# Kernel tuning notes

Hardware: AMD Instinct MI355X
Metric: run time of the kernel (lower is better)

## Reference

```python
import jax, jax.numpy as jnp
import numpy as np

B, SQ, SK, D = 4, 2048, 2048, 1024


def setup_inputs() -> dict:
    key = jax.random.key(0)
    ks = jax.random.split(key, 8)
    s = 1.0 / np.sqrt(D)
    return {
        "input_seq": jax.random.normal(ks[0], (B, SQ, D), jnp.float32),
        "condition_seq": jax.random.normal(ks[1], (B, SK, D), jnp.float32),
        "Wq": jax.random.normal(ks[2], (D, D), jnp.float32) * s,
        "bq": jnp.zeros((D,), jnp.float32),
        "Wk": jax.random.normal(ks[3], (D, D), jnp.float32) * s,
        "bk": jnp.zeros((D,), jnp.float32),
        "Wv": jax.random.normal(ks[4], (D, D), jnp.float32) * s,
        "bv": jnp.zeros((D,), jnp.float32),
    }


def reference(input_seq, condition_seq, Wq, bq, Wk, bk, Wv, bv):
    # Linear projections (torch Linear: x @ W.T + b)
    q = jnp.einsum("bsd,ed->bse", input_seq, Wq) + bq        # [B,SQ,D]
    k = jnp.einsum("btd,ed->bte", condition_seq, Wk) + bk    # [B,SK,D]
    v = jnp.einsum("btd,ed->bte", condition_seq, Wv) + bv    # [B,SK,D]
    # NOTE: original module omits the 1/sqrt(d) scaling — kept faithful.
    scores = jnp.einsum("bse,bte->bst", q, k)                # [B,SQ,SK]
    attn = jax.nn.softmax(scores, axis=-1)
    attended = jnp.einsum("bst,bte->bse", attn, v)           # [B,SQ,D]
    return attended
```

## Files before the change

### kernel.cpp

```cpp
#include <hip/hip_runtime.h>

using f32x4  = __attribute__((ext_vector_type(4))) float;
using bf16x8 = __attribute__((ext_vector_type(8))) __bf16;
using f16x8  = __attribute__((ext_vector_type(8))) _Float16;
using u16x4  = __attribute__((ext_vector_type(4))) unsigned short;
using u16x8  = __attribute__((ext_vector_type(8))) unsigned short;

constexpr int Bb = 4, SQn = 2048, SKn = 2048, Dd = 1024;

__device__ __forceinline__ unsigned fbitsu(float x){ union{float f;unsigned u;}c; c.f=x; return c.u; }
__device__ __forceinline__ float ubitsf(unsigned u){ union{unsigned u;float f;}c; c.u=u; return c.f; }
__device__ __forceinline__ unsigned short hi_trunc(float x){ return (unsigned short)(fbitsu(x)>>16); }
__device__ __forceinline__ unsigned short hi_rne(float x){ unsigned u=fbitsu(x); return (unsigned short)((u + 0x7FFFu + ((u>>16)&1u))>>16); }
__device__ __forceinline__ float from_hi(unsigned short h){ return ubitsf(((unsigned)h)<<16); }
__device__ __forceinline__ unsigned short h_rne(float x){ _Float16 h = (_Float16)x; return __builtin_bit_cast(unsigned short, h); }
__device__ __forceinline__ float h2f(unsigned short u){ return (float)__builtin_bit_cast(_Float16, u); }

template<int DT> __device__ __forceinline__ unsigned short cvt_rne(float x){ return DT ? h_rne(x) : hi_rne(x); }
template<int DT> __device__ __forceinline__ float cvt_f(unsigned short u){ return DT ? h2f(u) : from_hi(u); }

__device__ __forceinline__ f32x4 mfma_bf16(bf16x8 a, bf16x8 b, f32x4 c){
    return __builtin_amdgcn_mfma_f32_16x16x32_bf16(a, b, c, 0, 0, 0);
}
__device__ __forceinline__ f32x4 mfma_f16(u16x8 a, u16x8 b, f32x4 c){
    return __builtin_amdgcn_mfma_f32_16x16x32_f16(
        __builtin_bit_cast(f16x8, a), __builtin_bit_cast(f16x8, b), c, 0, 0, 0);
}
template<int DT>
__device__ __forceinline__ f32x4 mfma_u16(u16x8 a, u16x8 b, f32x4 c){
    if constexpr (DT) return mfma_f16(a, b, c);
    else return __builtin_amdgcn_mfma_f32_16x16x32_bf16(
        __builtin_bit_cast(bf16x8, a), __builtin_bit_cast(bf16x8, b), c, 0, 0, 0);
}

__device__ __forceinline__ void gload16(const void* g, void* l){
    __builtin_amdgcn_global_load_lds(
        (const __attribute__((address_space(1))) unsigned int*)g,
        (__attribute__((address_space(3))) unsigned int*)l, 16, 0, 0);
}

__device__ __forceinline__ void xcd_swz(int& bx, int& by){
    const int nx = gridDim.x, nwg = nx * gridDim.y;
    int l = by * nx + bx;
    l = (l & 7) * (nwg >> 3) + (l >> 3);
    bx = l % nx; by = l / nx;
}

__global__ __launch_bounds__(256)
void split2(const float* __restrict__ x, const float* __restrict__ c,
            unsigned short* __restrict__ xh, unsigned short* __restrict__ xl,
            unsigned short* __restrict__ ch, unsigned short* __restrict__ cl,
            int n4)
{
    const int stride = gridDim.x * 256;
    for (int i = blockIdx.x * 256 + threadIdx.x; i < 2 * n4; i += stride) {
        const bool second = (i >= n4);
        const int j = second ? i - n4 : i;
        const float* in = second ? c : x;
        unsigned short* hi = second ? ch : xh;
        unsigned short* lo = second ? cl : xl;
        float a[4]; *(float4*)a = *(const float4*)(in + (size_t)j * 4);
        u16x4 h, l;
#pragma unroll
        for (int r = 0; r < 4; ++r) {
            h[r] = h_rne(a[r]);
            l[r] = h_rne(a[r] - h2f(h[r]));
        }
        *(u16x4*)&hi[(size_t)j * 4] = h;
        *(u16x4*)&lo[(size_t)j * 4] = l;
    }
}

template<int TERMS, int BM_, int BN_, int BK_, int EPI, int DT>
__global__ __launch_bounds__(256, 2)
void gemm_tile(const unsigned short* __restrict__ Ahg, const unsigned short* __restrict__ Alg,
               const unsigned short* __restrict__ Bhg, const unsigned short* __restrict__ Blg,
               void* __restrict__ O0v, void* __restrict__ O1v,
               int M, int N, int K, long aBS, long bBS, long oBS)
{
    constexpr int ROWB = BK_ * 2;
    constexpr int RPC  = 1024 / ROWB;
    constexpr int CA   = BM_ / RPC;
    constexpr int CB   = BN_ / RPC;
    constexpr int AI   = BM_ / 32;
    constexpr int BJ   = BN_ / 32;
    constexpr int KH   = BK_ / 32;
    static_assert(CA % 4 == 0 && CB % 4 == 0, "chunks divisible by 4 waves");

    __shared__ __align__(16) unsigned short Ash[BM_*BK_], Bsh[BN_*BK_];
    __shared__ __align__(16) unsigned short Asl[TERMS>=2?BM_*BK_:8];
    __shared__ __align__(16) unsigned short Bsl[TERMS==3?BN_*BK_:8];

    const int z = blockIdx.z;
    Ahg += (size_t)z * aBS;
    Bhg += (size_t)z * bBS;
    if (TERMS >= 2) Alg += (size_t)z * aBS;
    if (TERMS == 3) Blg += (size_t)z * bBS;

    int bx = blockIdx.x, by = blockIdx.y;
    xcd_swz(bx, by);

    const int tid = threadIdx.x, lane = tid & 63, w = tid >> 6;
    const int wr = (w >> 1) * (BM_/2), wc = (w & 1) * (BN_/2);
    const int lr = lane & 15, lg = lane >> 4;
    const int m0 = by * BM_, n0 = bx * BN_;
    constexpr int rsh = (ROWB == 64) ? 2 : 3;
    const int rowc = lane >> rsh;
    const int colb = (lane & ((1 << rsh) - 1)) << 4;
    const size_t rsBy = (size_t)K * 2;

    f32x4 acc[AI][BJ] = {};

    for (int k0 = 0; k0 < K; k0 += BK_) {
#pragma unroll
        for (int c4 = 0; c4 < CA/4; ++c4) {
            const int c = c4*4 + w;
            const size_t go = (size_t)(m0 + c*RPC + rowc) * rsBy + (size_t)k0*2 + colb;
            gload16((const char*)Ahg + go, (char*)Ash + c*1024);
            if (TERMS >= 2) gload16((const char*)Alg + go, (char*)Asl + c*1024);
        }
#pragma unroll
        for (int c4 = 0; c4 < CB/4; ++c4) {
            const int c = c4*4 + w;
            const size_t go = (size_t)(n0 + c*RPC + rowc) * rsBy + (size_t)k0*2 + colb;
            gload16((const char*)Bhg + go, (char*)Bsh + c*1024);
            if (TERMS == 3) gload16((const char*)Blg + go, (char*)Bsl + c*1024);
        }
        __syncthreads();

#pragma unroll
        for (int kk = 0; kk < KH; ++kk) {
            u16x8 ah[AI], bh[BJ];
#pragma unroll
            for (int i = 0; i < AI; ++i) ah[i] = *(const u16x8*)&Ash[(wr + i*16 + lr)*BK_ + kk*32 + lg*8];
#pragma unroll
            for (int j = 0; j < BJ; ++j) bh[j] = *(const u16x8*)&Bsh[(wc + j*16 + lr)*BK_ + kk*32 + lg*8];
            if (TERMS == 3) {
                u16x8 al[AI], bl[BJ];
#pragma unroll
                for (int i = 0; i < AI; ++i) al[i] = *(const u16x8*)&Asl[(wr + i*16 + lr)*BK_ + kk*32 + lg*8];
#pragma unroll
                for (int j = 0; j < BJ; ++j) bl[j] = *(const u16x8*)&Bsl[(wc + j*16 + lr)*BK_ + kk*32 + lg*8];
#pragma unroll
                for (int i = 0; i < AI; ++i)
#pragma unroll
                    for (int j = 0; j < BJ; ++j) {
                        acc[i][j] = mfma_u16<DT>(ah[i], bh[j], acc[i][j]);
                        acc[i][j] = mfma_u16<DT>(ah[i], bl[j], acc[i][j]);
                        acc[i][j] = mfma_u16<DT>(al[i], bh[j], acc[i][j]);
                    }
            } else if (TERMS == 2) {
                u16x8 al[AI];
#pragma unroll
                for (int i = 0; i < AI; ++i) al[i] = *(const u16x8*)&Asl[(wr + i*16 + lr)*BK_ + kk*32 + lg*8];
#pragma unroll
                for (int i = 0; i < AI; ++i)
#pragma unroll
                    for (int j = 0; j < BJ; ++j) {
                        acc[i][j] = mfma_u16<DT>(ah[i], bh[j], acc[i][j]);
                        acc[i][j] = mfma_u16<DT>(al[i], bh[j], acc[i][j]);
                    }
            } else {
#pragma unroll
                for (int i = 0; i < AI; ++i)
#pragma unroll
                    for (int j = 0; j < BJ; ++j)
                        acc[i][j] = mfma_u16<DT>(ah[i], bh[j], acc[i][j]);
            }
        }
        __syncthreads();
    }

    if (EPI == 0) {
        float* C = (float*)O0v + (size_t)z * oBS;
#pragma unroll
        for (int j = 0; j < BJ; ++j) {
            const int col = n0 + wc + j*16 + lr;
#pragma unroll
            for (int i = 0; i < AI; ++i)
#pragma unroll
                for (int r = 0; r < 4; ++r)
                    C[(size_t)(m0 + wr + i*16 + lg*4 + r) * N + col] = acc[i][j][r];
        }
    } else {
        unsigned short* Chi = (unsigned short*)O0v + (size_t)z * oBS;
        unsigned short* Clo = (unsigned short*)O1v + (size_t)z * oBS;
#pragma unroll
        for (int j = 0; j < BJ; ++j) {
            const int col = n0 + wc + j*16 + lr;
#pragma unroll
            for (int i = 0; i < AI; ++i)
#pragma unroll
                for (int r = 0; r < 4; ++r) {
                    const size_t idx = (size_t)(m0 + wr + i*16 + lg*4 + r) * N + col;
                    const float v = acc[i][j][r];
                    const unsigned short h = cvt_rne<DT>(v);
                    Chi[idx] = h;
                    Clo[idx] = cvt_rne<DT>(v - cvt_f<DT>(h));
                }
        }
    }
}

template<int EPI>
__global__ __launch_bounds__(256, 2)
void gemm_mixed(const unsigned short* __restrict__ Ahg, const unsigned short* __restrict__ Alg,
                const float* __restrict__ Bw, const float* __restrict__ bias,
                unsigned short* __restrict__ O0, unsigned short* __restrict__ O1,
                int M, int N, int K)
{
    constexpr int BM_ = 128, BN_ = 128, BK_ = 32;
    __shared__ __align__(16) unsigned short Ash[BM_*BK_], Asl[BM_*BK_];
    __shared__ __align__(16) unsigned short Bsh[BN_*BK_];

    int bx = blockIdx.x, by = blockIdx.y;
    xcd_swz(bx, by);

    const int tid = threadIdx.x, lane = tid & 63, w = tid >> 6;
    const int wr = (w >> 1) * 64, wc = (w & 1) * 64;
    const int lr = lane & 15, lg = lane >> 4;
    const int m0 = by * BM_, n0 = bx * BN_;
    const int rowc = lane >> 2;
    const int colb = (lane & 3) << 4;
    const size_t rsBy = (size_t)K * 2;

    f32x4 acc[4][4] = {};

    for (int k0 = 0; k0 < K; k0 += BK_) {
        float4 bv[4];
#pragma unroll
        for (int u = 0; u < 4; ++u) {
            const int f = u*256 + tid;
            bv[u] = *(const float4*)(Bw + (size_t)(n0 + (f >> 3))*K + k0 + ((f & 7) << 2));
        }
        __syncthreads();

#pragma unroll
        for (int c4 = 0; c4 < 2; ++c4) {
            const int c = c4*4 + w;
            const size_t go = (size_t)(m0 + c*16 + rowc) * rsBy + (size_t)k0*2 + colb;
            gload16((const char*)Ahg + go, (char*)Ash + c*1024);
            gload16((const char*)Alg + go, (char*)Asl + c*1024);
        }
#pragma unroll
        for (int u = 0; u < 4; ++u) {
            const int f = u*256 + tid;
            const int row = f >> 3, ko = (f & 7) << 2;
            float b4[4]; *(float4*)b4 = bv[u];
            u16x4 bh;
#pragma unroll
            for (int r = 0; r < 4; ++r) bh[r] = h_rne(b4[r]);
            *(u16x4*)&Bsh[row*BK_ + ko] = bh;
        }
        __syncthreads();

        u16x8 ah[4], al[4], bh[4];
#pragma unroll
        for (int i = 0; i < 4; ++i) {
            ah[i] = *(const u16x8*)&Ash[(wr + i*16 + lr)*BK_ + lg*8];
            al[i] = *(const u16x8*)&Asl[(wr + i*16 + lr)*BK_ + lg*8];
        }
#pragma unroll
        for (int j = 0; j < 4; ++j) bh[j] = *(const u16x8*)&Bsh[(wc + j*16 + lr)*BK_ + lg*8];
#pragma unroll
        for (int i = 0; i < 4; ++i)
#pragma unroll
            for (int j = 0; j < 4; ++j) {
                acc[i][j] = mfma_f16(ah[i], bh[j], acc[i][j]);
                acc[i][j] = mfma_f16(al[i], bh[j], acc[i][j]);
            }
    }

#pragma unroll
    for (int j = 0; j < 4; ++j) {
        const int col = n0 + wc + j*16 + lr;
        const float bc = bias[col];
#pragma unroll
        for (int i = 0; i < 4; ++i) {
            if (EPI == 0) {
#pragma unroll
                for (int r = 0; r < 4; ++r) {
                    const int row = m0 + wr + i*16 + lg*4 + r;
                    const float v = acc[i][j][r] + bc;
                    const unsigned short h = h_rne(v);
                    O0[(size_t)row*N + col] = h;
                    O1[(size_t)row*N + col] = h_rne(v - h2f(h));
                }
            } else if (EPI == 2) {
#pragma unroll
                for (int r = 0; r < 4; ++r) {
                    const int row = m0 + wr + i*16 + lg*4 + r;
                    O0[(size_t)row*N + col] = h_rne(acc[i][j][r] + bc);
                }
            } else {
                const int row0 = m0 + wr + i*16 + lg*4;
                const int b = row0 >> 11, t0 = row0 & 2047;
                u16x4 pk;
#pragma unroll
                for (int r = 0; r < 4; ++r) pk[r] = h_rne(acc[i][j][r] + bc);
                *(u16x4*)&O0[(((size_t)b*Dd + col) << 11) + t0] = pk;
            }
        }
    }
}

template<int TERMS, int EPI>
__global__ __launch_bounds__(256, 2)
void gemm_proj(const float* __restrict__ A, const float* __restrict__ Bm,
               const float* __restrict__ bias,
               unsigned short* __restrict__ O0, unsigned short* __restrict__ O1,
               int M, int N, int K)
{
    constexpr int BM_ = 128, BN_ = 64, BK_ = 32;
    __shared__ __align__(16) unsigned short Ash[BM_*BK_], Bsh[BN_*BK_];
    __shared__ __align__(16) unsigned short Asl[TERMS==3?BM_*BK_:8], Bsl[TERMS==3?BN_*BK_:8];

    const int tid = threadIdx.x, lane = tid & 63, w = tid >> 6;
    const int wr = (w >> 1) * 64, wc = (w & 1) * 32;
    const int lr = lane & 15, lg = lane >> 4;
    const int m0 = blockIdx.y * BM_, n0 = blockIdx.x * BN_;

    f32x4 acc[4][2] = {};

    for (int k0 = 0; k0 < K; k0 += BK_) {
        float4 av[4], bv[2];
#pragma unroll
        for (int u = 0; u < 4; ++u) {
            const int f = u*256 + tid;
            av[u] = *(const float4*)(A + (size_t)(m0 + (f >> 3))*K + k0 + ((f & 7) << 2));
        }
#pragma unroll
        for (int u = 0; u < 2; ++u) {
            const int f = u*256 + tid;
            bv[u] = *(const float4*)(Bm + (size_t)(n0 + (f >> 3))*K + k0 + ((f & 7) << 2));
        }
        __syncthreads();
#pragma unroll
        for (int u = 0; u < 4; ++u) {
            const int f = u*256 + tid;
            const int row = f >> 3, ko = (f & 7) << 2;
            float a4[4]; *(float4*)a4 = av[u];
            u16x4 ah;
            if (TERMS == 3) {
                u16x4 al;
#pragma unroll
                for (int j = 0; j < 4; ++j) { ah[j] = hi_trunc(a4[j]); al[j] = hi_trunc(a4[j] - from_hi(ah[j])); }
                *(u16x4*)&Asl[row*BK_ + ko] = al;
            } else {
#pragma unroll
                for (int j = 0; j < 4; ++j) ah[j] = hi_rne(a4[j]);
            }
            *(u16x4*)&Ash[row*BK_ + ko] = ah;
        }
#pragma unroll
        for (int u = 0; u < 2; ++u) {
            const int f = u*256 + tid;
            const int row = f >> 3, ko = (f & 7) << 2;
            float b4[4]; *(float4*)b4 = bv[u];
            u16x4 bh;
            if (TERMS == 3) {
                u16x4 bl;
#pragma unroll
                for (int j = 0; j < 4; ++j) { bh[j] = hi_trunc(b4[j]); bl[j] = hi_trunc(b4[j] - from_hi(bh[j])); }
                *(u16x4*)&Bsl[row*BK_ + ko] = bl;
            } else {
#pragma unroll
                for (int j = 0; j < 4; ++j) bh[j] = hi_rne(b4[j]);
            }
            *(u16x4*)&Bsh[row*BK_ + ko] = bh;
        }
        __syncthreads();

        bf16x8 ah[4], bh[2];
#pragma unroll
        for (int i = 0; i < 4; ++i) ah[i] = *(const bf16x8*)&Ash[(wr + i*16 + lr)*BK_ + lg*8];
#pragma unroll
        for (int j = 0; j < 2; ++j) bh[j] = *(const bf16x8*)&Bsh[(wc + j*16 + lr)*BK_ + lg*8];
        if (TERMS == 3) {
            bf16x8 al[4], bl[2];
#pragma unroll
            for (int i = 0; i < 4; ++i) al[i] = *(const bf16x8*)&Asl[(wr + i*16 + lr)*BK_ + lg*8];
#pragma unroll
            for (int j = 0; j < 2; ++j) bl[j] = *(const bf16x8*)&Bsl[(wc + j*16 + lr)*BK_ + lg*8];
#pragma unroll
            for (int i = 0; i < 4; ++i)
#pragma unroll
                for (int j = 0; j < 2; ++j) {
                    acc[i][j] = mfma_bf16(ah[i], bh[j], acc[i][j]);
                    acc[i][j] = mfma_bf16(ah[i], bl[j], acc[i][j]);
                    acc[i][j] = mfma_bf16(al[i], bh[j], acc[i][j]);
                }
        } else {
#pragma unroll
            for (int i = 0; i < 4; ++i)
#pragma unroll
                for (int j = 0; j < 2; ++j)
                    acc[i][j] = mfma_bf16(ah[i], bh[j], acc[i][j]);
        }
        __syncthreads();
    }

#pragma unroll
    for (int j = 0; j < 2; ++j) {
        const int col = n0 + wc + j*16 + lr;
        const float bc = bias[col];
#pragma unroll
        for (int i = 0; i < 4; ++i) {
            if (EPI == 0) {
#pragma unroll
                for (int r = 0; r < 4; ++r) {
                    const int row = m0 + wr + i*16 + lg*4 + r;
                    const float v = acc[i][j][r] + bc;
                    const unsigned short h = h_rne(v);
                    O0[(size_t)row*N + col] = h;
                    O1[(size_t)row*N + col] = h_rne(v - h2f(h));
                }
            } else if (EPI == 2) {
#pragma unroll
                for (int r = 0; r < 4; ++r) {
                    const int row = m0 + wr + i*16 + lg*4 + r;
                    O0[(size_t)row*N + col] = h_rne(acc[i][j][r] + bc);
                }
            } else {
                const int row0 = m0 + wr + i*16 + lg*4;
                const int b = row0 >> 11, t0 = row0 & 2047;
                u16x4 pk;
#pragma unroll
                for (int r = 0; r < 4; ++r) pk[r] = h_rne(acc[i][j][r] + bc);
                *(u16x4*)&O0[(((size_t)b*Dd + col) << 11) + t0] = pk;
            }
        }
    }
}

__global__ __launch_bounds__(256)
void softmax_sp(unsigned short* __restrict__ Shi, const unsigned short* __restrict__ Slo)
{
    const int tid = threadIdx.x;
    unsigned short* ph = Shi + (size_t)blockIdx.x * SKn;
    const unsigned short* pl = Slo + (size_t)blockIdx.x * SKn;
    __shared__ float red[8];

    u16x4 h0 = *(const u16x4*)&ph[tid*4];
    u16x4 h1 = *(const u16x4*)&ph[1024 + tid*4];
    u16x4 l0 = *(const u16x4*)&pl[tid*4];
    u16x4 l1 = *(const u16x4*)&pl[1024 + tid*4];
    float v[8];
#pragma unroll
    for (int r = 0; r < 4; ++r) {
        v[r]   = h2f(h0[r]) + h2f(l0[r]);
        v[4+r] = h2f(h1[r]) + h2f(l1[r]);
    }
    float m = v[0];
#pragma unroll
    for (int r = 1; r < 8; ++r) m = fmaxf(m, v[r]);
#pragma unroll
    for (int o2 = 32; o2 > 0; o2 >>= 1) m = fmaxf(m, __shfl_down(m, o2));
    if ((tid & 63) == 0) red[tid >> 6] = m;
    __syncthreads();
    m = fmaxf(fmaxf(red[0],red[1]), fmaxf(red[2],red[3]));

    float e[8], s = 0.f;
#pragma unroll
    for (int r = 0; r < 8; ++r) { e[r] = __expf(v[r] - m); s += e[r]; }
#pragma unroll
    for (int o2 = 32; o2 > 0; o2 >>= 1) s += __shfl_down(s, o2);
    if ((tid & 63) == 0) red[4 + (tid >> 6)] = s;
    __syncthreads();
    const float inv = 1.f / ((red[4]+red[5])+(red[6]+red[7]));

    u16x4 p0, p1;
#pragma unroll
    for (int r = 0; r < 4; ++r) { p0[r] = h_rne(e[r]*inv); p1[r] = h_rne(e[4+r]*inv); }
    *(u16x4*)&ph[tid*4] = p0;
    *(u16x4*)&ph[1024 + tid*4] = p1;
}

extern "C" void kernel_launch(void* const* d_in, const int* in_sizes, int n_in,
                              void* d_out, int out_size, void* d_ws, size_t ws_size,
                              hipStream_t stream)
{
    const float* x  = (const float*)d_in[0];
    const float* c  = (const float*)d_in[1];
    const float* Wq = (const float*)d_in[2];
    const float* bq = (const float*)d_in[3];
    const float* Wk = (const float*)d_in[4];
    const float* bk = (const float*)d_in[5];
    const float* Wv = (const float*)d_in[6];
    const float* bv = (const float*)d_in[7];
    float* out = (float*)d_out;

    const size_t nQ = (size_t)Bb * SQn * Dd;
    const size_t sE = (size_t)SQn * SKn;
    unsigned short* Qh = (unsigned short*)d_ws;
    unsigned short* Ql = Qh + nQ;
    unsigned short* Kh = Ql + nQ;
    unsigned short* Kl = Kh + nQ;
    unsigned short* Vt = Kl + nQ;
    unsigned short* Shi = Vt + nQ;
    unsigned short* Slo = Shi + (size_t)Bb * sE;

    unsigned short* xh = Shi;
    unsigned short* xl = Shi + nQ;
    unsigned short* ch = Slo;
    unsigned short* cl = Slo + nQ;

    const size_t needB = (size_t)(Shi - Qh) * 2 + (size_t)Bb * sE * 2 * 2;
    const bool batched = ws_size >= needB;

    const dim3 blk(256);

    if (batched) {
        split2<<<dim3(4096), blk, 0, stream>>>(x, c, xh, xl, ch, cl, (int)(nQ/4));

        const dim3 gp(Dd/128, (Bb*SQn)/128);
        gemm_mixed<0><<<gp, blk, 0, stream>>>(xh, xl, Wq, bq, Qh, Ql, Bb*SQn, Dd, Dd);
        gemm_mixed<2><<<gp, blk, 0, stream>>>(ch, cl, Wk, bk, Kh, nullptr, Bb*SKn, Dd, Dd);
        gemm_mixed<1><<<gp, blk, 0, stream>>>(ch, cl, Wv, bv, Vt, nullptr, Bb*SKn, Dd, Dd);

        gemm_tile<2,128,128,32,1,1><<<dim3(SKn/128, SQn/128, Bb), blk, 0, stream>>>(
            Qh, Ql, Kh, nullptr, Shi, Slo, SQn, SKn, Dd,
            (long)SQn*Dd, (long)SKn*Dd, (long)sE);
        softmax_sp<<<dim3(Bb*SQn), blk, 0, stream>>>(Shi, Slo);
        gemm_tile<1,128,128,32,0,1><<<dim3(Dd/128, SQn/128, Bb), blk, 0, stream>>>(
            Shi, nullptr, Vt, nullptr, out, nullptr, SQn, Dd, SKn,
            (long)sE, (long)Dd*SKn, (long)SQn*Dd);
    } else {
        unsigned short* ShiF = Shi;
        unsigned short* SloF = Shi + sE;
        gemm_proj<3,0><<<dim3(Dd/64, (Bb*SQn)/128), blk, 0, stream>>>(x, Wq, bq, Qh, Ql, Bb*SQn, Dd, Dd);
        gemm_proj<3,2><<<dim3(Dd/64, (Bb*SKn)/128), blk, 0, stream>>>(c, Wk, bk, Kh, nullptr, Bb*SKn, Dd, Dd);
        gemm_proj<1,1><<<dim3(Dd/64, (Bb*SKn)/128), blk, 0, stream>>>(c, Wv, bv, Vt, nullptr, Bb*SKn, Dd, Dd);
        for (int b = 0; b < Bb; ++b) {
            const size_t qoff = (size_t)b * SQn * Dd;
            const size_t koff = (size_t)b * SKn * Dd;
            gemm_tile<2,128,64,32,1,1><<<dim3(SKn/64, SQn/128, 1), blk, 0, stream>>>(
                Qh+qoff, Ql+qoff, Kh+koff, nullptr, ShiF, SloF, SQn, SKn, Dd, 0, 0, 0);
            softmax_sp<<<dim3(SQn), blk, 0, stream>>>(ShiF, SloF);
            gemm_tile<1,64,64,32,0,1><<<dim3(Dd/64, SQn/64, 1), blk, 0, stream>>>(
                ShiF, nullptr, Vt+(size_t)b*Dd*SKn, nullptr, out+qoff, nullptr,
                SQn, Dd, SKn, 0, 0, 0);
        }
    }
}
```

Measured before the change: 315.6 us.

## Pre-convert projection weights to fp16 once and fuse K/V projections into one kernel

A new cvtW kernel converts Wq, Wk and Wv to fp16 once, into workspace space reused from the unused Kl buffer. The projection GEMMs then load B tiles with async global-to-LDS copies instead of reloading fp32 weights and converting them in every tile. The Q projection now goes through the generic gemm_tile with a new bias epilogue. The K and V projections are fused into one gemm_kv kernel that loads the split condition tiles once and feeds both weight matrices, which doubles the accumulator registers and may reduce occupancy.

```diff
diff --git a/kernel.cpp b/kernel.cpp
--- a/kernel.cpp
+++ b/kernel.cpp
@@ -71,10 +71,31 @@
     }
 }
 
+__global__ __launch_bounds__(256)
+void cvtW(const float* __restrict__ Wq, const float* __restrict__ Wk,
+          const float* __restrict__ Wv,
+          unsigned short* __restrict__ oq, unsigned short* __restrict__ ok,
+          unsigned short* __restrict__ ov, int n4)
+{
+    const int stride = gridDim.x * 256;
+    for (int i = blockIdx.x * 256 + threadIdx.x; i < 3 * n4; i += stride) {
+        const float* src; unsigned short* dst; int j = i;
+        if (j < n4)          { src = Wq; dst = oq; }
+        else if (j < 2*n4)   { src = Wk; dst = ok; j -= n4; }
+        else                 { src = Wv; dst = ov; j -= 2*n4; }
+        float a[4]; *(float4*)a = *(const float4*)(src + (size_t)j * 4);
+        u16x4 h;
+#pragma unroll
+        for (int r = 0; r < 4; ++r) h[r] = h_rne(a[r]);
+        *(u16x4*)&dst[(size_t)j * 4] = h;
+    }
+}
+
 template<int TERMS, int BM_, int BN_, int BK_, int EPI, int DT>
 __global__ __launch_bounds__(256, 2)
 void gemm_tile(const unsigned short* __restrict__ Ahg, const unsigned short* __restrict__ Alg,
                const unsigned short* __restrict__ Bhg, const unsigned short* __restrict__ Blg,
+               const float* __restrict__ bias,
                void* __restrict__ O0v, void* __restrict__ O1v,
                int M, int N, int K, long aBS, long bBS, long oBS)
 {
@@ -188,12 +209,13 @@
 #pragma unroll
         for (int j = 0; j < BJ; ++j) {
             const int col = n0 + wc + j*16 + lr;
+            const float bc = (EPI == 2) ? bias[col] : 0.f;
 #pragma unroll
             for (int i = 0; i < AI; ++i)
 #pragma unroll
                 for (int r = 0; r < 4; ++r) {
                     const size_t idx = (size_t)(m0 + wr + i*16 + lg*4 + r) * N + col;
-                    const float v = acc[i][j][r];
+                    const float v = acc[i][j][r] + bc;
                     const unsigned short h = cvt_rne<DT>(v);
                     Chi[idx] = h;
                     Clo[idx] = cvt_rne<DT>(v - cvt_f<DT>(h));
@@ -202,16 +224,16 @@
     }
 }
 
-template<int EPI>
 __global__ __launch_bounds__(256, 2)
-void gemm_mixed(const unsigned short* __restrict__ Ahg, const unsigned short* __restrict__ Alg,
-                const float* __restrict__ Bw, const float* __restrict__ bias,
-                unsigned short* __restrict__ O0, unsigned short* __restrict__ O1,
-                int M, int N, int K)
+void gemm_kv(const unsigned short* __restrict__ Ahg, const unsigned short* __restrict__ Alg,
+             const unsigned short* __restrict__ Wk16, const unsigned short* __restrict__ Wv16,
+             const float* __restrict__ bk, const float* __restrict__ bv,
+             unsigned short* __restrict__ Kh, unsigned short* __restrict__ Vt,
+             int M, int N, int K)
 {
     constexpr int BM_ = 128, BN_ = 128, BK_ = 32;
     __shared__ __align__(16) unsigned short Ash[BM_*BK_], Asl[BM_*BK_];
-    __shared__ __align__(16) unsigned short Bsh[BN_*BK_];
+    __shared__ __align__(16) unsigned short Bks[BN_*BK_], Bvs[BN_*BK_];
 
     int bx = blockIdx.x, by = blockIdx.y;
     xcd_swz(bx, by);
@@ -224,82 +246,63 @@
     const int colb = (lane & 3) << 4;
     const size_t rsBy = (size_t)K * 2;
 
-    f32x4 acc[4][4] = {};
+    f32x4 acck[4][4] = {}, accv[4][4] = {};
 
     for (int k0 = 0; k0 < K; k0 += BK_) {
-        float4 bv[4];
-#pragma unroll
-        for (int u = 0; u < 4; ++u) {
-            const int f = u*256 + tid;
-            bv[u] = *(const float4*)(Bw + (size_t)(n0 + (f >> 3))*K + k0 + ((f & 7) << 2));
-        }
-        __syncthreads();
-
 #pragma unroll
         for (int c4 = 0; c4 < 2; ++c4) {
             const int c = c4*4 + w;
-            const size_t go = (size_t)(m0 + c*16 + rowc) * rsBy + (size_t)k0*2 + colb;
-            gload16((const char*)Ahg + go, (char*)Ash + c*1024);
-            gload16((const char*)Alg + go, (char*)Asl + c*1024);
-        }
-#pragma unroll
-        for (int u = 0; u < 4; ++u) {
-            const int f = u*256 + tid;
-            const int row = f >> 3, ko = (f & 7) << 2;
-            float b4[4]; *(float4*)b4 = bv[u];
-            u16x4 bh;
-#pragma unroll
-            for (int r = 0; r < 4; ++r) bh[r] = h_rne(b4[r]);
-            *(u16x4*)&Bsh[row*BK_ + ko] = bh;
-        }
-        __syncthreads();
-
-        u16x8 ah[4], al[4], bh[4];
+            const size_t goA = (size_t)(m0 + c*16 + rowc) * rsBy + (size_t)k0*2 + colb;
+            gload16((const char*)Ahg + goA, (char*)Ash + c*1024);
+            gload16((const char*)Alg + goA, (char*)Asl + c*1024);
+            const size_t goB = (size_t)(n0 + c*16 + rowc) * rsBy + (size_t)k0*2 + colb;
+            gload16((const char*)Wk16 + goB, (char*)Bks + c*1024);
+            gload16((const char*)Wv16 + goB, (char*)Bvs + c*1024);
+        }
+        __syncthreads();
+
+        u16x8 ah[4], al[4], bf[4];
 #pragma unroll
         for (int i = 0; i < 4; ++i) {
             ah[i] = *(const u16x8*)&Ash[(wr + i*16 + lr)*BK_ + lg*8];
             al[i] = *(const u16x8*)&Asl[(wr + i*16 + lr)*BK_ + lg*8];
         }
 #pragma unroll
-        for (int j = 0; j < 4; ++j) bh[j] = *(const u16x8*)&Bsh[(wc + j*16 + lr)*BK_ + lg*8];
+        for (int j = 0; j < 4; ++j) bf[j] = *(const u16x8*)&Bks[(wc + j*16 + lr)*BK_ + lg*8];
 #pragma unroll
         for (int i = 0; i < 4; ++i)
 #pragma unroll
             for (int j = 0; j < 4; ++j) {
-                acc[i][j] = mfma_f16(ah[i], bh[j], acc[i][j]);
-                acc[i][j] = mfma_f16(al[i], bh[j], acc[i][j]);
+                acck[i][j] = mfma_f16(ah[i], bf[j], acck[i][j]);
+                acck[i][j] = mfma_f16(al[i], bf[j], acck[i][j]);
             }
+#pragma unroll
+        for (int j = 0; j < 4; ++j) bf[j] = *(const u16x8*)&Bvs[(wc + j*16 + lr)*BK_ + lg*8];
+#pragma unroll
+        for (int i = 0; i < 4; ++i)
+#pragma unroll
+            for (int j = 0; j < 4; ++j) {
+                accv[i][j] = mfma_f16(ah[i], bf[j], accv[i][j]);
+                accv[i][j] = mfma_f16(al[i], bf[j], accv[i][j]);
+            }
+        __syncthreads();
     }
 
 #pragma unroll
     for (int j = 0; j < 4; ++j) {
         const int col = n0 + wc + j*16 + lr;
-        const float bc = bias[col];
+        const float bck = bk[col], bcv = bv[col];
 #pragma unroll
         for (int i = 0; i < 4; ++i) {
-            if (EPI == 0) {
-#pragma unroll
-                for (int r = 0; r < 4; ++r) {
-                    const int row = m0 + wr + i*16 + lg*4 + r;
-                    const float v = acc[i][j][r] + bc;
-                    const unsigned short h = h_rne(v);
-                    O0[(size_t)row*N + col] = h;
-                    O1[(size_t)row*N + col] = h_rne(v - h2f(h));
-                }
-            } else if (EPI == 2) {
-#pragma unroll
-                for (int r = 0; r < 4; ++r) {
-                    const int row = m0 + wr + i*16 + lg*4 + r;
-                    O0[(size_t)row*N + col] = h_rne(acc[i][j][r] + bc);
-                }
-            } else {
-                const int row0 = m0 + wr + i*16 + lg*4;
-                const int b = row0 >> 11, t0 = row0 & 2047;
-                u16x4 pk;
-#pragma unroll
-                for (int r = 0; r < 4; ++r) pk[r] = h_rne(acc[i][j][r] + bc);
-                *(u16x4*)&O0[(((size_t)b*Dd + col) << 11) + t0] = pk;
-            }
+            const int row0 = m0 + wr + i*16 + lg*4;
+#pragma unroll
+            for (int r = 0; r < 4; ++r)
+                Kh[(size_t)(row0 + r)*N + col] = h_rne(acck[i][j][r] + bck);
+            const int b = row0 >> 11, t0 = row0 & 2047;
+            u16x4 pk;
+#pragma unroll
+            for (int r = 0; r < 4; ++r) pk[r] = h_rne(accv[i][j][r] + bcv);
+            *(u16x4*)&Vt[(((size_t)b*Dd + col) << 11) + t0] = pk;
         }
     }
 }
@@ -492,6 +495,7 @@
 
     const size_t nQ = (size_t)Bb * SQn * Dd;
     const size_t sE = (size_t)SQn * SKn;
+    const size_t nW = (size_t)Dd * Dd;
     unsigned short* Qh = (unsigned short*)d_ws;
     unsigned short* Ql = Qh + nQ;
     unsigned short* Kh = Ql + nQ;
@@ -500,6 +504,10 @@
     unsigned short* Shi = Vt + nQ;
     unsigned short* Slo = Shi + (size_t)Bb * sE;
 
+    unsigned short* Wq16 = Kl;
+    unsigned short* Wk16 = Kl + nW;
+    unsigned short* Wv16 = Kl + 2*nW;
+
     unsigned short* xh = Shi;
     unsigned short* xl = Shi + nQ;
     unsigned short* ch = Slo;
@@ -512,18 +520,19 @@
 
     if (batched) {
         split2<<<dim3(4096), blk, 0, stream>>>(x, c, xh, xl, ch, cl, (int)(nQ/4));
-
-        const dim3 gp(Dd/128, (Bb*SQn)/128);
-        gemm_mixed<0><<<gp, blk, 0, stream>>>(xh, xl, Wq, bq, Qh, Ql, Bb*SQn, Dd, Dd);
-        gemm_mixed<2><<<gp, blk, 0, stream>>>(ch, cl, Wk, bk, Kh, nullptr, Bb*SKn, Dd, Dd);
-        gemm_mixed<1><<<gp, blk, 0, stream>>>(ch, cl, Wv, bv, Vt, nullptr, Bb*SKn, Dd, Dd);
+        cvtW<<<dim3(1024), blk, 0, stream>>>(Wq, Wk, Wv, Wq16, Wk16, Wv16, (int)(nW/4));
+
+        gemm_tile<2,128,128,32,2,1><<<dim3(Dd/128, (Bb*SQn)/128), blk, 0, stream>>>(
+            xh, xl, Wq16, nullptr, bq, Qh, Ql, Bb*SQn, Dd, Dd, 0, 0, 0);
+        gemm_kv<<<dim3(Dd/128, (Bb*SKn)/128), blk, 0, stream>>>(
+            ch, cl, Wk16, Wv16, bk, bv, Kh, Vt, Bb*SKn, Dd, Dd);
 
         gemm_tile<2,128,128,32,1,1><<<dim3(SKn/128, SQn/128, Bb), blk, 0, stream>>>(
-            Qh, Ql, Kh, nullptr, Shi, Slo, SQn, SKn, Dd,
+            Qh, Ql, Kh, nullptr, nullptr, Shi, Slo, SQn, SKn, Dd,
             (long)SQn*Dd, (long)SKn*Dd, (long)sE);
         softmax_sp<<<dim3(Bb*SQn), blk, 0, stream>>>(Shi, Slo);
         gemm_tile<1,128,128,32,0,1><<<dim3(Dd/128, SQn/128, Bb), blk, 0, stream>>>(
-            Shi, nullptr, Vt, nullptr, out, nullptr, SQn, Dd, SKn,
+            Shi, nullptr, Vt, nullptr, nullptr, out, nullptr, SQn, Dd, SKn,
             (long)sE, (long)Dd*SKn, (long)SQn*Dd);
     } else {
         unsigned short* ShiF = Shi;
@@ -535,10 +544,10 @@
             const size_t qoff = (size_t)b * SQn * Dd;
             const size_t koff = (size_t)b * SKn * Dd;
             gemm_tile<2,128,64,32,1,1><<<dim3(SKn/64, SQn/128, 1), blk, 0, stream>>>(
-                Qh+qoff, Ql+qoff, Kh+koff, nullptr, ShiF, SloF, SQn, SKn, Dd, 0, 0, 0);
+                Qh+qoff, Ql+qoff, Kh+koff, nullptr, nullptr, ShiF, SloF, SQn, SKn, Dd, 0, 0, 0);
             softmax_sp<<<dim3(SQn), blk, 0, stream>>>(ShiF, SloF);
             gemm_tile<1,64,64,32,0,1><<<dim3(Dd/64, SQn/64, 1), blk, 0, stream>>>(
-                ShiF, nullptr, Vt+(size_t)b*Dd*SKn, nullptr, out+qoff, nullptr,
+                ShiF, nullptr, Vt+(size_t)b*Dd*SKn, nullptr, nullptr, out+qoff, nullptr,
                 SQn, Dd, SKn, 0, 0, 0);
         }
     }
```

New measurement: 287.2 us. 1.1x faster.
